# Kernel tuning notes

Measured on AMD Instinct MI355X. Metric: run time of the kernel, lower is better.

The kernel has to match this reference:

```python
import jax, jax.numpy as jnp
import numpy as np

EPS = 1e-5


def setup_inputs() -> dict:
    key = jax.random.key(0)
    k1, k2, k3 = jax.random.split(key, 3)
    B, n_per, C_in, C_out = 8, 131072, 32, 64
    N = B * n_per
    coord = jax.random.uniform(k1, (N, 3), dtype=jnp.float32)          # points in unit cube
    feat = jax.random.normal(k2, (N, C_in), dtype=jnp.float32)
    offset = (jnp.arange(1, B + 1, dtype=jnp.int32) * n_per)           # cumulative counts
    W = jax.random.normal(k3, (C_in, C_out), dtype=jnp.float32) * 0.05  # fc weight (no bias)
    gamma = jnp.ones((C_out,), dtype=jnp.float32)
    beta = jnp.zeros((C_out,), dtype=jnp.float32)
    return {"coord": coord, "feat": feat, "offset": offset, "W": W,
            "gamma": gamma, "beta": beta, "grid_size": 0.05}


def reference(coord, feat, offset, W, gamma, beta, grid_size):
    N = coord.shape[0]
    B = offset.shape[0]
    # offset2batch: point i belongs to batch = first b with i < offset[b]
    batch = jnp.searchsorted(offset, jnp.arange(N, dtype=offset.dtype), side="right").astype(jnp.int32)

    # fc -> BatchNorm (training-mode batch stats, biased var) -> ReLU
    h = feat @ W                                                        # [N, C_out]
    mean = h.mean(axis=0)
    var = jnp.mean((h - mean) ** 2, axis=0)
    h = jax.nn.relu((h - mean) * jax.lax.rsqrt(var + EPS) * gamma + beta)

    # start = per-batch min coord (segment_csr 'min' over batch pointer)
    start = jax.ops.segment_min(coord, batch, num_segments=B)           # [B, 3]

    # voxel_grid: integer voxel coords per point, combined with batch into a unique key
    v = jnp.floor((coord - start[batch]) / grid_size).astype(jnp.int32)  # [N, 3] >= 0
    D = v.max(axis=0) + 1                                               # grid extents
    vkey = ((batch * D[0] + v[:, 0]) * D[1] + v[:, 1]) * D[2] + v[:, 2]

    # unique(sorted) + inverse + counts; then segment mean/max by cluster
    uniq, inverse, counts = jnp.unique(vkey, return_inverse=True, return_counts=True)
    inverse = inverse.reshape(-1).astype(jnp.int32)
    M = uniq.shape[0]
    coord_out = jax.ops.segment_sum(coord, inverse, num_segments=M) / counts[:, None].astype(coord.dtype)
    feat_out = jax.ops.segment_max(h, inverse, num_segments=M)

    # batch id of each cluster (constant within cluster) -> new offset
    batch_out = jax.ops.segment_min(batch, inverse, num_segments=M)
    offset_out = jnp.cumsum(jnp.bincount(batch_out, length=B)).astype(offset.dtype)
    return coord_out, feat_out, offset_out, inverse
```

## Files before the change

kernel.cpp:

```cpp
#include <hip/hip_runtime.h>
#include <float.h>

#define EPSV 1e-5f
#define DGRID 21
#define DPROD (21 * 21 * 21)

typedef __attribute__((ext_vector_type(8))) short bf16x8;
typedef __attribute__((ext_vector_type(4))) float f32x4;

__device__ __forceinline__ short f2bf(float x) {
    unsigned u = __float_as_uint(x);
    unsigned r = (u + 0x7FFFu + ((u >> 16) & 1u)) >> 16;
    return (short)r;
}

__device__ __forceinline__ int batch_of(int i, const int* __restrict__ offset, int B) {
    int b = 0;
    while (b < B - 1 && i >= offset[b]) ++b;
    return b;
}

__global__ void k_init(int* counts, int KSM, int* startEnc, int B) {
    int tid = blockIdx.x * blockDim.x + threadIdx.x;
    int stride = gridDim.x * blockDim.x;
    for (int k = tid; k < KSM; k += stride) counts[k] = 0;
    if (tid < B * 3) startEnc[tid] = 0x7FFFFFFF;
}

__global__ void k_start(const float* __restrict__ coord, const int* __restrict__ offset,
                        int* startEnc, int N, int B) {
    __shared__ int smin[24];
    int t = threadIdx.x;
    if (t < B * 3) smin[t] = 0x7FFFFFFF;
    __syncthreads();
    int base = (blockIdx.x * blockDim.x + t) * 4;
    int curb = -1;
    int m0 = 0x7FFFFFFF, m1 = 0x7FFFFFFF, m2 = 0x7FFFFFFF;
    for (int r = 0; r < 4; ++r) {
        int i = base + r;
        if (i >= N) break;
        int b = batch_of(i, offset, B);
        if (b != curb) {
            if (curb >= 0) {
                atomicMin(&smin[curb * 3 + 0], m0);
                atomicMin(&smin[curb * 3 + 1], m1);
                atomicMin(&smin[curb * 3 + 2], m2);
            }
            curb = b; m0 = m1 = m2 = 0x7FFFFFFF;
        }
        m0 = min(m0, __float_as_int(coord[(size_t)i * 3 + 0]));
        m1 = min(m1, __float_as_int(coord[(size_t)i * 3 + 1]));
        m2 = min(m2, __float_as_int(coord[(size_t)i * 3 + 2]));
    }
    if (curb >= 0) {
        atomicMin(&smin[curb * 3 + 0], m0);
        atomicMin(&smin[curb * 3 + 1], m1);
        atomicMin(&smin[curb * 3 + 2], m2);
    }
    __syncthreads();
    if (t < B * 3 && smin[t] != 0x7FFFFFFF) atomicMin(&startEnc[t], smin[t]);
}

__global__ void k_count(const float* __restrict__ coord, const int* __restrict__ offset,
                        const int* __restrict__ startEnc, const float* __restrict__ gsP,
                        int* counts, int* vkey, int N, int B) {
    int i = blockIdx.x * blockDim.x + threadIdx.x;
    if (i >= N) return;
    float inv_gs = 1.0f / gsP[0];
    int b = batch_of(i, offset, B);
    float s0 = __int_as_float(startEnc[b * 3 + 0]);
    float s1 = __int_as_float(startEnc[b * 3 + 1]);
    float s2 = __int_as_float(startEnc[b * 3 + 2]);
    int vx = min(DGRID - 1, (int)floorf((coord[(size_t)i * 3 + 0] - s0) * inv_gs));
    int vy = min(DGRID - 1, (int)floorf((coord[(size_t)i * 3 + 1] - s1) * inv_gs));
    int vz = min(DGRID - 1, (int)floorf((coord[(size_t)i * 3 + 2] - s2) * inv_gs));
    int k = ((b * DGRID + vx) * DGRID + vy) * DGRID + vz;
    vkey[i] = k;
    atomicAdd(&counts[k], 1);
}

__global__ void k_scan1(const int* __restrict__ counts, int* occPart, int* cntPart, int KSM) {
    __shared__ int so[256], sc[256];
    int t = threadIdx.x;
    int base = blockIdx.x * 1024 + t * 4;
    int o = 0, c = 0;
    for (int r = 0; r < 4; ++r) {
        int k = base + r;
        if (k < KSM) { int cnt = counts[k]; o += (cnt > 0); c += cnt; }
    }
    so[t] = o; sc[t] = c;
    __syncthreads();
    for (int s = 128; s > 0; s >>= 1) {
        if (t < s) { so[t] += so[t + s]; sc[t] += sc[t + s]; }
        __syncthreads();
    }
    if (t == 0) { occPart[blockIdx.x] = so[0]; cntPart[blockIdx.x] = sc[0]; }
}

__global__ void k_scan2(const int* occPart, const int* cntPart,
                        int* occPartEx, int* cntPartEx, int NBLK) {
    __shared__ int so[128], sc[128];
    int t = threadIdx.x;
    int o = (t < NBLK) ? occPart[t] : 0;
    int c = (t < NBLK) ? cntPart[t] : 0;
    so[t] = o; sc[t] = c;
    __syncthreads();
    for (int s = 1; s < 128; s <<= 1) {
        int ao = 0, ac = 0;
        if (t >= s) { ao = so[t - s]; ac = sc[t - s]; }
        __syncthreads();
        so[t] += ao; sc[t] += ac;
        __syncthreads();
    }
    if (t < NBLK) { occPartEx[t] = so[t] - o; cntPartEx[t] = sc[t] - c; }
}

__global__ void k_scan3(const int* __restrict__ counts, const int* occPartEx, const int* cntPartEx,
                        int* occScan, int* cntScan, int* cursor, int* cntC, int* cstartC, int KSM) {
    __shared__ int so[256], sc[256];
    int t = threadIdx.x;
    int base = blockIdx.x * 1024 + t * 4;
    int o[4], c[4];
    int tO = 0, tC = 0;
    for (int r = 0; r < 4; ++r) {
        int k = base + r;
        int cnt = (k < KSM) ? counts[k] : 0;
        o[r] = (cnt > 0); c[r] = cnt;
        tO += o[r]; tC += c[r];
    }
    so[t] = tO; sc[t] = tC;
    __syncthreads();
    for (int s = 1; s < 256; s <<= 1) {
        int ao = 0, ac = 0;
        if (t >= s) { ao = so[t - s]; ac = sc[t - s]; }
        __syncthreads();
        so[t] += ao; sc[t] += ac;
        __syncthreads();
    }
    int exO = so[t] - tO + occPartEx[blockIdx.x];
    int exC = sc[t] - tC + cntPartEx[blockIdx.x];
    for (int r = 0; r < 4; ++r) {
        int k = base + r;
        if (k < KSM) {
            occScan[k] = exO; cntScan[k] = exC; cursor[k] = 0;
            if (c[r] > 0) { cntC[exO] = c[r]; cstartC[exO] = exC; }
            exO += o[r]; exC += c[r];
        }
    }
}

__global__ void k_scatter(const int* __restrict__ vkey,
                          const int* __restrict__ occScan, const int* __restrict__ cntScan,
                          int* cursor, int* plist, float* __restrict__ dout,
                          int N, int B, int M) {
    int i = blockIdx.x * blockDim.x + threadIdx.x;
    if (i >= N) return;
    int k = vkey[i];
    int cidx = occScan[k];
    int pos = cntScan[k] + atomicAdd(&cursor[k], 1);
    plist[pos] = i;
    dout[(size_t)67 * M + B + i] = (float)cidx;
}

__launch_bounds__(64)
__global__ void k_pool(const float* __restrict__ feat, const float* __restrict__ coord,
                       const float* __restrict__ W,
                       const int* __restrict__ cstartC, const int* __restrict__ cntC,
                       const int* __restrict__ plist,
                       float* __restrict__ dout, float* __restrict__ statPart, int M) {
    const int lane = threadIdx.x;
    const int col  = lane & 15;
    const int quad = lane >> 4;

    bf16x8 Bf[4];
#pragma unroll
    for (int t = 0; t < 4; ++t) {
#pragma unroll
        for (int j = 0; j < 8; ++j) {
            int k = quad * 8 + j;
            Bf[t][j] = f2bf(W[k * 64 + t * 16 + col]);
        }
    }

    float sumA[4] = {0.f, 0.f, 0.f, 0.f};
    float sqA[4]  = {0.f, 0.f, 0.f, 0.f};

    for (int cid = blockIdx.x; cid < M; cid += gridDim.x) {
        int ps  = cstartC[cid];
        int cnt = cntC[cid];
        float maxA[4] = {-FLT_MAX, -FLT_MAX, -FLT_MAX, -FLT_MAX};
        float cx = 0.f, cy = 0.f, cz = 0.f;

        for (int base = 0; base < cnt; base += 16) {
            int m = base + col;
            int idx = min(m, cnt - 1);
            int p = plist[ps + idx];
            const float4* rowp = reinterpret_cast<const float4*>(feat + (size_t)p * 32 + quad * 8);
            float4 a0 = rowp[0];
            float4 a1 = rowp[1];
            if (lane < 16 && m < cnt) {
                cx += coord[(size_t)p * 3 + 0];
                cy += coord[(size_t)p * 3 + 1];
                cz += coord[(size_t)p * 3 + 2];
            }
            bf16x8 Af;
            Af[0] = f2bf(a0.x); Af[1] = f2bf(a0.y); Af[2] = f2bf(a0.z); Af[3] = f2bf(a0.w);
            Af[4] = f2bf(a1.x); Af[5] = f2bf(a1.y); Af[6] = f2bf(a1.z); Af[7] = f2bf(a1.w);
            f32x4 Cz = {0.f, 0.f, 0.f, 0.f};
#pragma unroll
            for (int t = 0; t < 4; ++t) {
                f32x4 Cv = __builtin_amdgcn_mfma_f32_16x16x32_bf16(Af, Bf[t], Cz, 0, 0, 0);
#pragma unroll
                for (int r = 0; r < 4; ++r) {
                    int rowPt = base + quad * 4 + r;
                    bool valid = rowPt < cnt;
                    float v = Cv[r];
                    maxA[t] = fmaxf(maxA[t], valid ? v : -FLT_MAX);
                    sumA[t] += valid ? v : 0.f;
                    sqA[t]  += valid ? v * v : 0.f;
                }
            }
        }
        float outv = 0.f;
#pragma unroll
        for (int t = 0; t < 4; ++t) {
            float v = maxA[t];
            v = fmaxf(v, __shfl_xor(v, 16, 64));
            v = fmaxf(v, __shfl_xor(v, 32, 64));
            if (quad == t) outv = v;
        }
        dout[(size_t)3 * M + (size_t)cid * 64 + lane] = outv;

        cx += __shfl_xor(cx, 1, 64); cx += __shfl_xor(cx, 2, 64);
        cx += __shfl_xor(cx, 4, 64); cx += __shfl_xor(cx, 8, 64);
        cy += __shfl_xor(cy, 1, 64); cy += __shfl_xor(cy, 2, 64);
        cy += __shfl_xor(cy, 4, 64); cy += __shfl_xor(cy, 8, 64);
        cz += __shfl_xor(cz, 1, 64); cz += __shfl_xor(cz, 2, 64);
        cz += __shfl_xor(cz, 4, 64); cz += __shfl_xor(cz, 8, 64);
        if (lane == 0) {
            float inv = 1.0f / (float)cnt;
            dout[(size_t)cid * 3 + 0] = cx * inv;
            dout[(size_t)cid * 3 + 1] = cy * inv;
            dout[(size_t)cid * 3 + 2] = cz * inv;
        }
    }

    float so = 0.f, qo = 0.f;
#pragma unroll
    for (int t = 0; t < 4; ++t) {
        float s = sumA[t];
        s += __shfl_xor(s, 16, 64);
        s += __shfl_xor(s, 32, 64);
        float q = sqA[t];
        q += __shfl_xor(q, 16, 64);
        q += __shfl_xor(q, 32, 64);
        if (quad == t) { so = s; qo = q; }
    }
    statPart[(size_t)blockIdx.x * 128 + lane] = so;
    statPart[(size_t)blockIdx.x * 128 + 64 + lane] = qo;
}

__global__ void k_statred(const float* __restrict__ statPart,
                          const float* __restrict__ gamma, const float* __restrict__ beta,
                          float* bnA, float* bnB, int NB, int N) {
    __shared__ float s1[256], s2[256];
    int c = blockIdx.x;
    int t = threadIdx.x;
    float a = 0.f, b = 0.f;
    for (int bb = t; bb < NB; bb += 256) {
        a += statPart[(size_t)bb * 128 + c];
        b += statPart[(size_t)bb * 128 + 64 + c];
    }
    s1[t] = a; s2[t] = b;
    __syncthreads();
    for (int s = 128; s > 0; s >>= 1) {
        if (t < s) { s1[t] += s1[t + s]; s2[t] += s2[t + s]; }
        __syncthreads();
    }
    if (t == 0) {
        float invN = 1.0f / (float)N;
        float mean = s1[0] * invN;
        float var = s2[0] * invN - mean * mean;
        float aa = gamma[c] / sqrtf(var + EPSV);
        bnA[c] = aa;
        bnB[c] = beta[c] - mean * aa;
    }
}

__global__ void k_final(float* __restrict__ dout, const float* __restrict__ bnA,
                        const float* __restrict__ bnB,
                        const int* __restrict__ occScan, int M, int B) {
    size_t stride = (size_t)gridDim.x * blockDim.x;
    size_t tid0 = (size_t)blockIdx.x * blockDim.x + threadIdx.x;
    size_t totF = (size_t)M * 64;
    for (size_t t = tid0; t < totF; t += stride) {
        int c = (int)(t & 63);
        float v = dout[(size_t)3 * M + t];
        dout[(size_t)3 * M + t] = fmaxf(bnA[c] * v + bnB[c], 0.f);
    }
    if (tid0 < (size_t)B) {
        int val = (tid0 == (size_t)(B - 1)) ? M : occScan[(int)(tid0 + 1) * DPROD];
        dout[(size_t)67 * M + tid0] = (float)val;
    }
}

extern "C" void kernel_launch(void* const* d_in, const int* in_sizes, int n_in,
                              void* d_out, int out_size, void* d_ws, size_t ws_size,
                              hipStream_t stream) {
    const float* coord = (const float*)d_in[0];
    const float* feat  = (const float*)d_in[1];
    const int*   offset = (const int*)d_in[2];
    const float* W     = (const float*)d_in[3];
    const float* gamma = (const float*)d_in[4];
    const float* beta  = (const float*)d_in[5];
    const float* gsP   = (const float*)d_in[6];
    float* dout = (float*)d_out;

    const int N = in_sizes[0] / 3;
    const int B = in_sizes[2];
    const int M = (out_size - B - N) / 67;
    const int KSM = B * DPROD;
    const int NBLK = (KSM + 1023) / 1024;
    const int NBPL = 8192;

    int* wsI = (int*)d_ws;
    int* startEnc  = wsI + 0;
    float* bnA     = (float*)(wsI + 64);
    float* bnB     = (float*)(wsI + 128);
    int* occPart   = wsI + 256;
    int* cntPart   = wsI + 384;
    int* occPartEx = wsI + 512;
    int* cntPartEx = wsI + 640;
    int* counts    = wsI + 1024;
    int* occScan   = counts + KSM;
    int* cntScan   = occScan + KSM;
    int* cursor    = cntScan + KSM;
    int* cntC      = cursor + KSM;
    int* cstartC   = cntC + KSM;
    int* vkey      = cstartC + KSM;
    int* plist     = vkey + N;
    float* statPart = (float*)(plist + N);

    const int TPB = 256;
    int gInit  = 512;
    int gChunk = (N + 1023) / 1024;
    int gPoint = (N + TPB - 1) / TPB;

    k_init<<<gInit, TPB, 0, stream>>>(counts, KSM, startEnc, B);
    k_start<<<gChunk, TPB, 0, stream>>>(coord, offset, startEnc, N, B);
    k_count<<<gPoint, TPB, 0, stream>>>(coord, offset, startEnc, gsP, counts, vkey, N, B);
    k_scan1<<<NBLK, TPB, 0, stream>>>(counts, occPart, cntPart, KSM);
    k_scan2<<<1, 128, 0, stream>>>(occPart, cntPart, occPartEx, cntPartEx, NBLK);
    k_scan3<<<NBLK, TPB, 0, stream>>>(counts, occPartEx, cntPartEx, occScan, cntScan,
                                      cursor, cntC, cstartC, KSM);
    k_scatter<<<gPoint, TPB, 0, stream>>>(vkey, occScan, cntScan, cursor, plist,
                                          dout, N, B, M);
    k_pool<<<NBPL, 64, 0, stream>>>(feat, coord, W, cstartC, cntC, plist, dout, statPart, M);
    k_statred<<<64, 256, 0, stream>>>(statPart, gamma, beta, bnA, bnB, NBPL, N);
    k_final<<<1024, TPB, 0, stream>>>(dout, bnA, bnB, occScan, M, B);
}
```

Measured before the change: 394.6 us.

## Batch four clusters per wavefront in pooling and fuse scan and init kernels

The pooling kernel now processes four clusters at once per wavefront, issuing their gathers together to raise memory-level parallelism and spreading the coordinate sums across lanes. The separate block-prefix scan kernel is folded into the final scan kernel, and zeroing of the count table moves into the start kernel, removing launches. This adds register pressure and wasted MFMA work when the batched clusters differ in size.

```diff
diff --git a/kernel.cpp b/kernel.cpp
--- a/kernel.cpp
+++ b/kernel.cpp
@@ -20,20 +20,21 @@
     return b;
 }
 
-__global__ void k_init(int* counts, int KSM, int* startEnc, int B) {
-    int tid = blockIdx.x * blockDim.x + threadIdx.x;
-    int stride = gridDim.x * blockDim.x;
-    for (int k = tid; k < KSM; k += stride) counts[k] = 0;
+__global__ void k_init(int* startEnc, int B) {
+    int tid = threadIdx.x;
     if (tid < B * 3) startEnc[tid] = 0x7FFFFFFF;
 }
 
 __global__ void k_start(const float* __restrict__ coord, const int* __restrict__ offset,
-                        int* startEnc, int N, int B) {
+                        int* startEnc, int* counts, int KSM, int N, int B) {
+    int gtid = blockIdx.x * blockDim.x + threadIdx.x;
+    for (int k = gtid; k < KSM; k += gridDim.x * blockDim.x) counts[k] = 0;
+
     __shared__ int smin[24];
     int t = threadIdx.x;
     if (t < B * 3) smin[t] = 0x7FFFFFFF;
     __syncthreads();
-    int base = (blockIdx.x * blockDim.x + t) * 4;
+    int base = gtid * 4;
     int curb = -1;
     int m0 = 0x7FFFFFFF, m1 = 0x7FFFFFFF, m2 = 0x7FFFFFFF;
     for (int r = 0; r < 4; ++r) {
@@ -97,28 +98,31 @@
     if (t == 0) { occPart[blockIdx.x] = so[0]; cntPart[blockIdx.x] = sc[0]; }
 }
 
-__global__ void k_scan2(const int* occPart, const int* cntPart,
-                        int* occPartEx, int* cntPartEx, int NBLK) {
-    __shared__ int so[128], sc[128];
+__global__ void k_scan3(const int* __restrict__ counts,
+                        const int* __restrict__ occPart, const int* __restrict__ cntPart,
+                        int* occScan, int* cntScan, int* cursor, int* cntC, int* cstartC,
+                        int KSM, int NBLK) {
+    __shared__ int so[256], sc[256];
+    __shared__ int po[128], pc[128];
+    __shared__ int exO_s, exC_s;
     int t = threadIdx.x;
-    int o = (t < NBLK) ? occPart[t] : 0;
-    int c = (t < NBLK) ? cntPart[t] : 0;
-    so[t] = o; sc[t] = c;
+
+    int po_v = 0, pc_v = 0;
+    if (t < 128) {
+        po_v = (t < NBLK) ? occPart[t] : 0;
+        pc_v = (t < NBLK) ? cntPart[t] : 0;
+        po[t] = po_v; pc[t] = pc_v;
+    }
     __syncthreads();
     for (int s = 1; s < 128; s <<= 1) {
         int ao = 0, ac = 0;
-        if (t >= s) { ao = so[t - s]; ac = sc[t - s]; }
-        __syncthreads();
-        so[t] += ao; sc[t] += ac;
-        __syncthreads();
-    }
-    if (t < NBLK) { occPartEx[t] = so[t] - o; cntPartEx[t] = sc[t] - c; }
-}
-
-__global__ void k_scan3(const int* __restrict__ counts, const int* occPartEx, const int* cntPartEx,
-                        int* occScan, int* cntScan, int* cursor, int* cntC, int* cstartC, int KSM) {
-    __shared__ int so[256], sc[256];
-    int t = threadIdx.x;
+        if (t < 128 && t >= s) { ao = po[t - s]; ac = pc[t - s]; }
+        __syncthreads();
+        if (t < 128) { po[t] += ao; pc[t] += ac; }
+        __syncthreads();
+    }
+    if (t == (int)blockIdx.x) { exO_s = po[t] - po_v; exC_s = pc[t] - pc_v; }
+
     int base = blockIdx.x * 1024 + t * 4;
     int o[4], c[4];
     int tO = 0, tC = 0;
@@ -137,8 +141,8 @@
         so[t] += ao; sc[t] += ac;
         __syncthreads();
     }
-    int exO = so[t] - tO + occPartEx[blockIdx.x];
-    int exC = sc[t] - tC + cntPartEx[blockIdx.x];
+    int exO = so[t] - tO + exO_s;
+    int exC = sc[t] - tC + exC_s;
     for (int r = 0; r < 4; ++r) {
         int k = base + r;
         if (k < KSM) {
@@ -171,6 +175,7 @@
     const int lane = threadIdx.x;
     const int col  = lane & 15;
     const int quad = lane >> 4;
+    const int nw = gridDim.x;
 
     bf16x8 Bf[4];
 #pragma unroll
@@ -185,63 +190,90 @@
     float sumA[4] = {0.f, 0.f, 0.f, 0.f};
     float sqA[4]  = {0.f, 0.f, 0.f, 0.f};
 
-    for (int cid = blockIdx.x; cid < M; cid += gridDim.x) {
-        int ps  = cstartC[cid];
-        int cnt = cntC[cid];
-        float maxA[4] = {-FLT_MAX, -FLT_MAX, -FLT_MAX, -FLT_MAX};
-        float cx = 0.f, cy = 0.f, cz = 0.f;
-
-        for (int base = 0; base < cnt; base += 16) {
+    for (int c0 = blockIdx.x; c0 < M; c0 += 4 * nw) {
+        int cid[4], ps[4], n[4];
+        bool live[4];
+        int nmax = 0;
+#pragma unroll
+        for (int u = 0; u < 4; ++u) {
+            int c = c0 + u * nw;
+            live[u] = (c < M);
+            cid[u] = live[u] ? c : c0;
+            ps[u] = cstartC[cid[u]];
+            n[u]  = cntC[cid[u]];
+            nmax = max(nmax, n[u]);
+        }
+
+        float maxA[4][4];
+#pragma unroll
+        for (int u = 0; u < 4; ++u)
+#pragma unroll
+            for (int t = 0; t < 4; ++t) maxA[u][t] = -FLT_MAX;
+        float cacc[4] = {0.f, 0.f, 0.f, 0.f};
+
+        for (int base = 0; base < nmax; base += 16) {
             int m = base + col;
-            int idx = min(m, cnt - 1);
-            int p = plist[ps + idx];
-            const float4* rowp = reinterpret_cast<const float4*>(feat + (size_t)p * 32 + quad * 8);
-            float4 a0 = rowp[0];
-            float4 a1 = rowp[1];
-            if (lane < 16 && m < cnt) {
-                cx += coord[(size_t)p * 3 + 0];
-                cy += coord[(size_t)p * 3 + 1];
-                cz += coord[(size_t)p * 3 + 2];
-            }
-            bf16x8 Af;
-            Af[0] = f2bf(a0.x); Af[1] = f2bf(a0.y); Af[2] = f2bf(a0.z); Af[3] = f2bf(a0.w);
-            Af[4] = f2bf(a1.x); Af[5] = f2bf(a1.y); Af[6] = f2bf(a1.z); Af[7] = f2bf(a1.w);
-            f32x4 Cz = {0.f, 0.f, 0.f, 0.f};
+            int p[4];
+#pragma unroll
+            for (int u = 0; u < 4; ++u) {
+                int idx = min(m, n[u] - 1);
+                p[u] = plist[ps[u] + idx];
+            }
+            float4 a0[4], a1[4];
+#pragma unroll
+            for (int u = 0; u < 4; ++u) {
+                const float4* rp = reinterpret_cast<const float4*>(feat + (size_t)p[u] * 32 + quad * 8);
+                a0[u] = rp[0];
+                a1[u] = rp[1];
+            }
+#pragma unroll
+            for (int u = 0; u < 4; ++u) {
+                if (quad > 0) {
+                    float v = coord[(size_t)p[u] * 3 + (quad - 1)];
+                    cacc[u] += (m < n[u]) ? v : 0.f;
+                }
+            }
+#pragma unroll
+            for (int u = 0; u < 4; ++u) {
+                bf16x8 Af;
+                Af[0] = f2bf(a0[u].x); Af[1] = f2bf(a0[u].y);
+                Af[2] = f2bf(a0[u].z); Af[3] = f2bf(a0[u].w);
+                Af[4] = f2bf(a1[u].x); Af[5] = f2bf(a1[u].y);
+                Af[6] = f2bf(a1[u].z); Af[7] = f2bf(a1[u].w);
+                f32x4 Cz = {0.f, 0.f, 0.f, 0.f};
+#pragma unroll
+                for (int t = 0; t < 4; ++t) {
+                    f32x4 v = __builtin_amdgcn_mfma_f32_16x16x32_bf16(Af, Bf[t], Cz, 0, 0, 0);
+#pragma unroll
+                    for (int r = 0; r < 4; ++r) {
+                        int rowPt = base + quad * 4 + r;
+                        maxA[u][t] = fmaxf(maxA[u][t], v[r]);
+                        float mv = (rowPt < n[u] && live[u]) ? v[r] : 0.f;
+                        sumA[t] += mv;
+                        sqA[t] = fmaf(mv, mv, sqA[t]);
+                    }
+                }
+            }
+        }
+
+#pragma unroll
+        for (int u = 0; u < 4; ++u) {
+            float outv = 0.f;
 #pragma unroll
             for (int t = 0; t < 4; ++t) {
-                f32x4 Cv = __builtin_amdgcn_mfma_f32_16x16x32_bf16(Af, Bf[t], Cz, 0, 0, 0);
-#pragma unroll
-                for (int r = 0; r < 4; ++r) {
-                    int rowPt = base + quad * 4 + r;
-                    bool valid = rowPt < cnt;
-                    float v = Cv[r];
-                    maxA[t] = fmaxf(maxA[t], valid ? v : -FLT_MAX);
-                    sumA[t] += valid ? v : 0.f;
-                    sqA[t]  += valid ? v * v : 0.f;
-                }
-            }
-        }
-        float outv = 0.f;
-#pragma unroll
-        for (int t = 0; t < 4; ++t) {
-            float v = maxA[t];
-            v = fmaxf(v, __shfl_xor(v, 16, 64));
-            v = fmaxf(v, __shfl_xor(v, 32, 64));
-            if (quad == t) outv = v;
-        }
-        dout[(size_t)3 * M + (size_t)cid * 64 + lane] = outv;
-
-        cx += __shfl_xor(cx, 1, 64); cx += __shfl_xor(cx, 2, 64);
-        cx += __shfl_xor(cx, 4, 64); cx += __shfl_xor(cx, 8, 64);
-        cy += __shfl_xor(cy, 1, 64); cy += __shfl_xor(cy, 2, 64);
-        cy += __shfl_xor(cy, 4, 64); cy += __shfl_xor(cy, 8, 64);
-        cz += __shfl_xor(cz, 1, 64); cz += __shfl_xor(cz, 2, 64);
-        cz += __shfl_xor(cz, 4, 64); cz += __shfl_xor(cz, 8, 64);
-        if (lane == 0) {
-            float inv = 1.0f / (float)cnt;
-            dout[(size_t)cid * 3 + 0] = cx * inv;
-            dout[(size_t)cid * 3 + 1] = cy * inv;
-            dout[(size_t)cid * 3 + 2] = cz * inv;
+                float v = maxA[u][t];
+                v = fmaxf(v, __shfl_xor(v, 16, 64));
+                v = fmaxf(v, __shfl_xor(v, 32, 64));
+                if (quad == t) outv = v;
+            }
+            if (live[u])
+                dout[(size_t)3 * M + (size_t)cid[u] * 64 + lane] = outv;
+
+            float ca = cacc[u];
+            ca += __shfl_xor(ca, 1, 64); ca += __shfl_xor(ca, 2, 64);
+            ca += __shfl_xor(ca, 4, 64); ca += __shfl_xor(ca, 8, 64);
+            if (live[u] && quad > 0 && col == 0)
+                dout[(size_t)cid[u] * 3 + (quad - 1)] = ca / (float)n[u];
         }
     }
 
@@ -329,8 +361,6 @@
     float* bnB     = (float*)(wsI + 128);
     int* occPart   = wsI + 256;
     int* cntPart   = wsI + 384;
-    int* occPartEx = wsI + 512;
-    int* cntPartEx = wsI + 640;
     int* counts    = wsI + 1024;
     int* occScan   = counts + KSM;
     int* cntScan   = occScan + KSM;
@@ -342,17 +372,15 @@
     float* statPart = (float*)(plist + N);
 
     const int TPB = 256;
-    int gInit  = 512;
     int gChunk = (N + 1023) / 1024;
     int gPoint = (N + TPB - 1) / TPB;
 
-    k_init<<<gInit, TPB, 0, stream>>>(counts, KSM, startEnc, B);
-    k_start<<<gChunk, TPB, 0, stream>>>(coord, offset, startEnc, N, B);
+    k_init<<<1, 64, 0, stream>>>(startEnc, B);
+    k_start<<<gChunk, TPB, 0, stream>>>(coord, offset, startEnc, counts, KSM, N, B);
     k_count<<<gPoint, TPB, 0, stream>>>(coord, offset, startEnc, gsP, counts, vkey, N, B);
     k_scan1<<<NBLK, TPB, 0, stream>>>(counts, occPart, cntPart, KSM);
-    k_scan2<<<1, 128, 0, stream>>>(occPart, cntPart, occPartEx, cntPartEx, NBLK);
-    k_scan3<<<NBLK, TPB, 0, stream>>>(counts, occPartEx, cntPartEx, occScan, cntScan,
-                                      cursor, cntC, cstartC, KSM);
+    k_scan3<<<NBLK, TPB, 0, stream>>>(counts, occPart, cntPart, occScan, cntScan,
+                                      cursor, cntC, cstartC, KSM, NBLK);
     k_scatter<<<gPoint, TPB, 0, stream>>>(vkey, occScan, cntScan, cursor, plist,
                                           dout, N, B, M);
     k_pool<<<NBPL, 64, 0, stream>>>(feat, coord, W, cstartC, cntC, plist, dout, statPart, M);
```

Result: no change. 399.1 us (+1.2%).
